# Kernel optimization log

Measured on AMD Instinct MI355X. Metric: run time of the kernel, lower is better.

The kernel has to match this reference:

```python
import jax, jax.numpy as jnp
import numpy as np

B, H, W, C = 16, 56, 56, 384
NH, WS = 12, 7
N = WS * WS
NW = (H // WS) * (W // WS)
SHIFTS = (0, WS // 2)
HD = C // NH
SCALE = HD ** -0.5


def _rel_idx():
    ch, cw = np.meshgrid(np.arange(WS), np.arange(WS), indexing='ij')
    cf = np.stack([ch.ravel(), cw.ravel()])            # (2, N)
    rc = cf[:, :, None] - cf[:, None, :]               # (2, N, N)
    rc = rc.transpose(1, 2, 0).copy()
    rc[:, :, 0] += WS - 1
    rc[:, :, 1] += WS - 1
    rc[:, :, 0] *= 2 * WS - 1
    return rc.sum(-1).astype(np.int32)                 # (N, N)


def _attn_mask(shift):
    img = np.zeros((H, W))
    sl = (slice(0, -WS), slice(-WS, -shift), slice(-shift, None))
    cnt = 0
    for hs in sl:
        for ws_ in sl:
            img[hs, ws_] = cnt
            cnt += 1
    mw = img.reshape(H // WS, WS, W // WS, WS).transpose(0, 2, 1, 3).reshape(-1, N)
    d = mw[:, None, :] - mw[:, :, None]
    return np.where(d != 0, -100.0, 0.0).astype(np.float32)  # (NW, N, N)


def setup_inputs() -> dict:
    key = jax.random.key(0)
    ks = jax.random.split(key, 8)
    p = lambda k, shape: (jax.random.normal(k, shape, jnp.float32) * 0.02)
    return dict(
        x=jax.random.normal(ks[0], (B, H, W, C), jnp.float32),
        attn_mask=jnp.asarray(_attn_mask(SHIFTS[1])),
        rel_idx=jnp.asarray(_rel_idx()),
        norm1_g=jnp.ones((2, C), jnp.float32),
        norm1_b=jnp.zeros((2, C), jnp.float32),
        qkv_w=p(ks[1], (2, 3 * C, C)),
        qkv_b=jnp.zeros((2, 3 * C), jnp.float32),
        rpb=p(ks[2], (2, (2 * WS - 1) ** 2, NH)),
        proj_w=p(ks[3], (2, C, C)),
        proj_b=jnp.zeros((2, C), jnp.float32),
        norm2_g=jnp.ones((2, C), jnp.float32),
        norm2_b=jnp.zeros((2, C), jnp.float32),
        fc1_w=p(ks[4], (2, 4 * C, C)),
        fc1_b=jnp.zeros((2, 4 * C), jnp.float32),
        fc2_w=p(ks[5], (2, C, 4 * C)),
        fc2_b=jnp.zeros((2, C), jnp.float32),
    )


def _ln(x, g, b):
    m = x.mean(-1, keepdims=True)
    v = x.var(-1, keepdims=True)
    return (x - m) * jax.lax.rsqrt(v + 1e-5) * g + b


def _partition(x):
    # (B,H,W,C) -> (B*nW, N, C)
    x = x.reshape(B, H // WS, WS, W // WS, WS, C)
    return x.transpose(0, 1, 3, 2, 4, 5).reshape(-1, N, C)


def _reverse(w):
    # (B*nW, N, C) -> (B,H,W,C)
    w = w.reshape(B, H // WS, W // WS, WS, WS, C)
    return w.transpose(0, 1, 3, 2, 4, 5).reshape(B, H, W, C)


def reference(x, attn_mask, rel_idx, norm1_g, norm1_b, qkv_w, qkv_b, rpb,
              proj_w, proj_b, norm2_g, norm2_b, fc1_w, fc1_b, fc2_w, fc2_b):
    for i, shift in enumerate(SHIFTS):
        shortcut = x.reshape(B, H * W, C)
        xn = _ln(shortcut, norm1_g[i], norm1_b[i]).reshape(B, H, W, C)
        if shift > 0:
            xn = jnp.roll(xn, (-shift, -shift), (1, 2))
        xw = _partition(xn)                               # (B_, N, C)
        qkv = xw @ qkv_w[i].T + qkv_b[i]                  # (B_, N, 3C)
        qkv = qkv.reshape(-1, N, 3, NH, HD).transpose(2, 0, 3, 1, 4)
        q, k, v = qkv[0], qkv[1], qkv[2]                  # (B_, NH, N, HD)
        attn = jnp.einsum('bhnd,bhmd->bhnm', q * SCALE, k)
        bias = rpb[i][rel_idx.reshape(-1)].reshape(N, N, NH).transpose(2, 0, 1)
        attn = attn + bias[None]
        if shift > 0:
            attn = attn.reshape(B, NW, NH, N, N) + attn_mask[None, :, None]
            attn = attn.reshape(-1, NH, N, N)
        attn = jax.nn.softmax(attn, axis=-1)
        out = jnp.einsum('bhnm,bhmd->bhnd', attn, v)
        out = out.transpose(0, 2, 1, 3).reshape(-1, N, C)
        out = out @ proj_w[i].T + proj_b[i]
        sx = _reverse(out)
        if shift > 0:
            sx = jnp.roll(sx, (shift, shift), (1, 2))
        x = shortcut + sx.reshape(B, H * W, C)
        h = jax.nn.gelu(_ln(x, norm2_g[i], norm2_b[i]) @ fc1_w[i].T + fc1_b[i],
                        approximate=False)
        x = x + (h @ fc2_w[i].T + fc2_b[i])
        x = x.reshape(B, H, W, C)
    return x
```

## Files before the change

### kernel.cpp

```cpp
#include <hip/hip_runtime.h>
#include <math.h>

typedef unsigned short u16;
typedef unsigned int   u32;
typedef __attribute__((ext_vector_type(4))) float f32x4;
typedef __attribute__((ext_vector_type(8))) short bf16x8;

#define M_TOK 50176
#define CDIM  384

__device__ __forceinline__ u16 f2b(float f){
  union { float f; u32 u; } v; v.f = f;
  u32 r = v.u + 0x7fffu + ((v.u >> 16) & 1u);
  return (u16)(r >> 16);
}
__device__ __forceinline__ u32 pack2(float a, float b){
  return (u32)f2b(a) | ((u32)f2b(b) << 16);
}

__device__ __forceinline__ void gload_lds16(const u16* g, u16* l){
  __builtin_amdgcn_global_load_lds((const __attribute__((address_space(1))) u32*)g,
                                   (__attribute__((address_space(3))) u32*)l, 16, 0, 0);
}

__global__ void cvtw(const float* __restrict__ in, u16* __restrict__ out, int n4){
  int i = blockIdx.x * 256 + threadIdx.x;
  if (i < n4){
    float4 v = ((const float4*)in)[i];
    uint2 o; o.x = pack2(v.x, v.y); o.y = pack2(v.z, v.w);
    ((uint2*)out)[i] = o;
  }
}

__global__ __launch_bounds__(256) void ln_kernel(
    const float* __restrict__ x, const float* __restrict__ g,
    const float* __restrict__ b, u16* __restrict__ out, int ntok)
{
  int wave = threadIdx.x >> 6, lane = threadIdx.x & 63;
  for (long t = blockIdx.x * 4 + wave; t < ntok; t += (long)gridDim.x * 4){
    const float* xr = x + t * CDIM;
    float v[6]; float s = 0.f, ss = 0.f;
    #pragma unroll
    for (int j = 0; j < 6; ++j){ v[j] = xr[j*64 + lane]; s += v[j]; ss += v[j]*v[j]; }
    #pragma unroll
    for (int o = 32; o >= 1; o >>= 1){ s += __shfl_xor(s, o); ss += __shfl_xor(ss, o); }
    float mean = s * (1.f/384.f);
    float var  = ss * (1.f/384.f) - mean*mean;
    float rs   = rsqrtf(var + 1e-5f);
    #pragma unroll
    for (int j = 0; j < 6; ++j){
      int c = j*64 + lane;
      out[t*CDIM + c] = f2b((v[j] - mean) * rs * g[c] + b[c]);
    }
  }
}

template<int EPI>
__global__ __launch_bounds__(256, 4) void gemm_bt(
    const u16* __restrict__ A, const u16* __restrict__ Wt,
    const float* __restrict__ bias, const float* __restrict__ resid,
    void* __restrict__ outp, int M, int N, int K)
{
  __shared__ __align__(16) u16 smem[16384];
  const int tid  = threadIdx.x;
  const int wave = tid >> 6, lane = tid & 63;
  const int nbn  = N >> 7;
  const int cpx  = gridDim.x >> 3;
  const int sid  = (blockIdx.x & 7) * cpx + (blockIdx.x >> 3);
  const int bm = sid / nbn, bn = sid % nbn;
  const int wr = wave >> 1, wc = wave & 1;
  const int l15 = lane & 15, l4 = lane >> 4;
  const int srow = tid >> 2, sch = tid & 3;

  f32x4 acc[4][4] = {};

  auto STAGE = [&](int buf, int kt){
    u16* lAp = smem + buf*4096;
    u16* lBp = smem + 8192 + buf*4096;
    #pragma unroll
    for (int it = 0; it < 2; ++it){
      int row = it*64 + srow;
      int chs = sch ^ ((srow >> 1) & 3);
      const u16* ga = A  + (size_t)(bm*128 + row) * K + kt + chs*8;
      const u16* gb = Wt + (size_t)(bn*128 + row) * K + kt + chs*8;
      gload_lds16(ga, &lAp[(it*256 + wave*64) * 8]);
      gload_lds16(gb, &lBp[(it*256 + wave*64) * 8]);
    }
  };

  const int NK = K >> 5;
  STAGE(0, 0);

  int cur = 0;
  for (int ki = 0; ki < NK; ++ki){
    if (ki + 1 < NK){
      STAGE(cur ^ 1, (ki + 1) * 32);
      asm volatile("s_waitcnt vmcnt(4)" ::: "memory");
    } else {
      asm volatile("s_waitcnt vmcnt(0)" ::: "memory");
    }
    __builtin_amdgcn_s_barrier();
    const u16* lAp = smem + cur*4096;
    const u16* lBp = smem + 8192 + cur*4096;
    bf16x8 af[4], bfr[4];
    const int rc = (l4 ^ ((l15 >> 1) & 3)) * 8;
    #pragma unroll
    for (int mi = 0; mi < 4; ++mi)
      af[mi] = *(const bf16x8*)&lAp[(wr*64 + mi*16 + l15)*32 + rc];
    #pragma unroll
    for (int ni = 0; ni < 4; ++ni)
      bfr[ni] = *(const bf16x8*)&lBp[(wc*64 + ni*16 + l15)*32 + rc];
    #pragma unroll
    for (int mi = 0; mi < 4; ++mi)
      #pragma unroll
      for (int ni = 0; ni < 4; ++ni)
        acc[mi][ni] = __builtin_amdgcn_mfma_f32_16x16x32_bf16(af[mi], bfr[ni], acc[mi][ni], 0, 0, 0);
    __builtin_amdgcn_s_barrier();
    cur ^= 1;
  }

  if (EPI == 2){
    #pragma unroll
    for (int ni = 0; ni < 4; ++ni){
      int col = bn*128 + wc*64 + ni*16 + l15;
      float bb = bias[col];
      #pragma unroll
      for (int mi = 0; mi < 4; ++mi){
        int row0 = bm*128 + wr*64 + mi*16 + l4*4;
        #pragma unroll
        for (int r = 0; r < 4; ++r){
          long off = (long)(row0 + r) * N + col;
          ((float*)outp)[off] = resid[off] + acc[mi][ni][r] + bb;
        }
      }
    }
  } else {
    #pragma unroll
    for (int ni = 0; ni < 4; ++ni){
      int colL = wc*64 + ni*16 + l15;
      float bb = bias[bn*128 + colL];
      int colS = colL ^ (l4*16);
      #pragma unroll
      for (int mi = 0; mi < 4; ++mi){
        int rowL = wr*64 + mi*16 + l4*4;
        #pragma unroll
        for (int r = 0; r < 4; ++r){
          float v = acc[mi][ni][r] + bb;
          if (EPI == 1) v = 0.5f * v * (1.f + erff(v * 0.70710678118654752f));
          smem[(rowL + r)*128 + colS] = f2b(v);
        }
      }
    }
    __syncthreads();
    const u32* eb = (const u32*)smem;
    u32* og = (u32*)outp;
    const int nW = N >> 1;
    #pragma unroll
    for (int it = 0; it < 32; ++it){
      int row = wave*32 + it;
      u32 w = eb[row*64 + (lane ^ (((row >> 2) & 3) * 8))];
      __builtin_nontemporal_store(w, &og[(size_t)(bm*128 + row) * nW + bn*64 + lane]);
    }
  }
}

__global__ void build_btbl(const float* __restrict__ rpb, const int* __restrict__ ridx,
                           float* __restrict__ btbl){
  int q = blockIdx.x & 63, h = blockIdx.x >> 6;
  int l = threadIdx.x;
  float v = -1e9f;
  if (q < 49){
    int key = (l & 3) * 16 + (l >> 2);
    if (key < 49) v = rpb[ridx[q*49 + key] * 12 + h];
  }
  btbl[(h*64 + q)*64 + l] = v;
}

template<int SHIFT>
__global__ __launch_bounds__(64) void attn_mfma(
    const u16* __restrict__ qkv,
    const float* __restrict__ btbl,
    u16* __restrict__ attn_out)
{
  __shared__ __align__(16) u16 p_lds[64*72];
  __shared__ __align__(16) u16 vt_lds[32*72];
  __shared__ int tok_lds[64];
  __shared__ int rid_lds[64];

  const int bid = blockIdx.x;
  const int h   = bid % 12;
  const int win = bid / 12;
  const int b   = win >> 6, wl = win & 63;
  const int wy  = wl >> 3,  wx = wl & 7;
  const int lane = threadIdx.x;
  const int l15 = lane & 15, l4 = lane >> 4;

  auto tokof = [&](int n)->int{
    int r = (n * 9363) >> 16;
    int c = n - r * 7;
    int hh = wy*7 + r + SHIFT; if (hh >= 56) hh -= 56;
    int ww = wx*7 + c + SHIFT; if (ww >= 56) ww -= 56;
    return b*3136 + hh*56 + ww;
  };

  {
    const int n  = lane;
    const int nc = n < 49 ? n : 48;
    const int t  = tokof(nc);
    tok_lds[n] = t;
    if (SHIFT){
      int r = (nc * 9363) >> 16, c = nc - r*7;
      int gh = wy*7 + r, gw = wx*7 + c;
      int rh = gh <= 48 ? 0 : (gh <= 52 ? 1 : 2);
      int rw = gw <= 48 ? 0 : (gw <= 52 ? 1 : 2);
      rid_lds[n] = rh*3 + rw;
    }
    const uint4* vp = (const uint4*)(qkv + (size_t)t*1152 + 768 + h*32);
    u32 w[16];
    #pragma unroll
    for (int j4 = 0; j4 < 4; ++j4){
      uint4 u = vp[j4];
      w[j4*4+0]=u.x; w[j4*4+1]=u.y; w[j4*4+2]=u.z; w[j4*4+3]=u.w;
    }
    if (n >= 49){
      #pragma unroll
      for (int j = 0; j < 16; ++j) w[j] = 0;
    }
    #pragma unroll
    for (int j = 0; j < 16; ++j){
      vt_lds[(2*j  )*72 + n] = (u16)(w[j] & 0xffffu);
      vt_lds[(2*j+1)*72 + n] = (u16)(w[j] >> 16);
    }
  }

  bf16x8 qa[4], kb[4];
  #pragma unroll
  for (int mi = 0; mi < 4; ++mi){
    int row = mi*16 + l15; int t = tokof(row < 49 ? row : 48);
    qa[mi] = *(const bf16x8*)(qkv + (size_t)t*1152 + h*32 + l4*8);
  }
  #pragma unroll
  for (int ni = 0; ni < 4; ++ni){
    int row = ni*16 + l15; int t = tokof(row < 49 ? row : 48);
    kb[ni] = *(const bf16x8*)(qkv + (size_t)t*1152 + 384 + h*32 + l4*8);
  }
  f32x4 s[4][4] = {};
  #pragma unroll
  for (int mi = 0; mi < 4; ++mi)
    #pragma unroll
    for (int ni = 0; ni < 4; ++ni)
      s[mi][ni] = __builtin_amdgcn_mfma_f32_16x16x32_bf16(qa[mi], kb[ni], s[mi][ni], 0, 0, 0);

  __syncthreads();

  int rid_k[4];
  if (SHIFT){
    #pragma unroll
    for (int ni = 0; ni < 4; ++ni) rid_k[ni] = rid_lds[ni*16 + l15];
  }

  const float* bt = btbl + h*4096;
  float den[4][4];
  #pragma unroll
  for (int mi = 0; mi < 4; ++mi){
    #pragma unroll
    for (int r = 0; r < 4; ++r){
      int q = mi*16 + l4*4 + r;
      f32x4 bq = *(const f32x4*)(bt + q*64 + l15*4);
      int ridq = 0;
      if (SHIFT) ridq = rid_lds[q];
      #pragma unroll
      for (int ni = 0; ni < 4; ++ni){
        float v = s[mi][ni][r] * 0.17677669529663687f + bq[ni];
        if (SHIFT) v += (ridq == rid_k[ni]) ? 0.f : -100.f;
        s[mi][ni][r] = v;
      }
      float m0 = fmaxf(fmaxf(s[mi][0][r], s[mi][1][r]), fmaxf(s[mi][2][r], s[mi][3][r]));
      #pragma unroll
      for (int o = 1; o <= 8; o <<= 1) m0 = fmaxf(m0, __shfl_xor(m0, o));
      float d0 = 0.f;
      #pragma unroll
      for (int ni = 0; ni < 4; ++ni){
        float e = __expf(s[mi][ni][r] - m0);
        s[mi][ni][r] = e; d0 += e;
      }
      #pragma unroll
      for (int o = 1; o <= 8; o <<= 1) d0 += __shfl_xor(d0, o);
      den[mi][r] = d0;
    }
  }

  #pragma unroll
  for (int mi = 0; mi < 4; ++mi)
    #pragma unroll
    for (int r = 0; r < 4; ++r){
      int q = mi*16 + l4*4 + r;
      #pragma unroll
      for (int ni = 0; ni < 4; ++ni)
        p_lds[q*72 + ni*16 + l15] = f2b(s[mi][ni][r]);
    }

  __syncthreads();

  f32x4 o2[4][2] = {};
  #pragma unroll
  for (int ks = 0; ks < 2; ++ks){
    bf16x8 vb[2];
    #pragma unroll
    for (int ni = 0; ni < 2; ++ni)
      vb[ni] = *(const bf16x8*)&vt_lds[(ni*16 + l15)*72 + ks*32 + l4*8];
    #pragma unroll
    for (int mi = 0; mi < 4; ++mi){
      bf16x8 pa = *(const bf16x8*)&p_lds[(mi*16 + l15)*72 + ks*32 + l4*8];
      #pragma unroll
      for (int ni = 0; ni < 2; ++ni)
        o2[mi][ni] = __builtin_amdgcn_mfma_f32_16x16x32_bf16(pa, vb[ni], o2[mi][ni], 0, 0, 0);
    }
  }

  #pragma unroll
  for (int mi = 0; mi < 4; ++mi){
    #pragma unroll
    for (int r = 0; r < 4; ++r){
      int q = mi*16 + l4*4 + r;
      if (q < 49){
        float inv = 1.f / den[mi][r];
        long t = tok_lds[q];
        #pragma unroll
        for (int ni = 0; ni < 2; ++ni){
          int d = ni*16 + l15;
          attn_out[t*384 + h*32 + d] = f2b(o2[mi][ni][r] * inv);
        }
      }
    }
  }
}

extern "C" void kernel_launch(void* const* d_in, const int* in_sizes, int n_in,
                              void* d_out, int out_size, void* d_ws, size_t ws_size,
                              hipStream_t stream)
{
  const float* x_in   = (const float*)d_in[0];
  const int*   relidx = (const int*)d_in[2];
  const float* n1g    = (const float*)d_in[3];
  const float* n1b    = (const float*)d_in[4];
  const float* qkvw   = (const float*)d_in[5];
  const float* qkvb   = (const float*)d_in[6];
  const float* rpb    = (const float*)d_in[7];
  const float* pw     = (const float*)d_in[8];
  const float* pb     = (const float*)d_in[9];
  const float* n2g    = (const float*)d_in[10];
  const float* n2b    = (const float*)d_in[11];
  const float* f1w    = (const float*)d_in[12];
  const float* f1b    = (const float*)d_in[13];
  const float* f2w    = (const float*)d_in[14];
  const float* f2bb   = (const float*)d_in[15];
  float* xout = (float*)d_out;

  char* ws = (char*)d_ws;
  u16* wqkv  = (u16*)ws; ws += (size_t)2*1152*384*2;
  u16* wproj = (u16*)ws; ws += (size_t)2*384*384*2;
  u16* wfc1  = (u16*)ws; ws += (size_t)2*1536*384*2;
  u16* wfc2  = (u16*)ws; ws += (size_t)2*384*1536*2;
  u16* bufA  = (u16*)ws; ws += (size_t)M_TOK*1536*2;
  u16* bufB  = (u16*)ws; ws += (size_t)M_TOK*384*2;
  float* btbl = (float*)(bufA + (size_t)M_TOK*1152);

  {
    int n;
    n = 2*1152*384;  cvtw<<<dim3((n/4+255)/256), dim3(256), 0, stream>>>(qkvw, wqkv, n/4);
    n = 2*384*384;   cvtw<<<dim3((n/4+255)/256), dim3(256), 0, stream>>>(pw,   wproj, n/4);
    n = 2*1536*384;  cvtw<<<dim3((n/4+255)/256), dim3(256), 0, stream>>>(f1w,  wfc1, n/4);
    n = 2*384*1536;  cvtw<<<dim3((n/4+255)/256), dim3(256), 0, stream>>>(f2w,  wfc2, n/4);
  }

  for (int i = 0; i < 2; ++i){
    const float* xi = (i == 0) ? x_in : xout;
    ln_kernel<<<dim3(2048), dim3(256), 0, stream>>>(xi, n1g + i*384, n1b + i*384, bufB, M_TOK);
    gemm_bt<0><<<dim3(3528), dim3(256), 0, stream>>>(
        bufB, wqkv + (size_t)i*1152*384, qkvb + i*1152, nullptr, bufA, M_TOK, 1152, 384);
    build_btbl<<<dim3(768), dim3(64), 0, stream>>>(rpb + (size_t)i*169*12, relidx, btbl);
    if (i == 0)
      attn_mfma<0><<<dim3(12288), dim3(64), 0, stream>>>(bufA, btbl, bufB);
    else
      attn_mfma<3><<<dim3(12288), dim3(64), 0, stream>>>(bufA, btbl, bufB);
    gemm_bt<2><<<dim3(1176), dim3(256), 0, stream>>>(
        bufB, wproj + (size_t)i*384*384, pb + i*384, xi, xout, M_TOK, 384, 384);
    ln_kernel<<<dim3(2048), dim3(256), 0, stream>>>(xout, n2g + i*384, n2b + i*384, bufB, M_TOK);
    gemm_bt<1><<<dim3(4704), dim3(256), 0, stream>>>(
        bufB, wfc1 + (size_t)i*1536*384, f1b + i*1536, nullptr, bufA, M_TOK, 1536, 384);
    gemm_bt<2><<<dim3(1176), dim3(256), 0, stream>>>(
        bufA, wfc2 + (size_t)i*384*1536, f2bb + i*384, xout, xout, M_TOK, 384, 1536);
  }
  (void)in_sizes; (void)n_in; (void)out_size; (void)ws_size;
}
```

Before: 965.0 us.

## Enlarge GEMM tile to 256x128 with triple-buffered LDS pipeline

Doubles the GEMM M-tile to 256 rows (8x4 MFMA accumulators per wave) and moves from double to triple buffering of the K-slices, with adjusted vmcnt waits. It also fixes the XCD block remap for grids not divisible by 8, halves all GEMM grid sizes, and splits the bf16 epilogue into two 128-row passes through LDS. The intent is better operand reuse per global load and deeper load latency hiding. In exchange it uses more registers and LDS, so occupancy drops (launch bounds lowered to 2 blocks per CU) and fewer workgroups are launched.

```diff
diff --git a/kernel.cpp b/kernel.cpp
--- a/kernel.cpp
+++ b/kernel.cpp
@@ -56,67 +56,76 @@
 }
 
 template<int EPI>
-__global__ __launch_bounds__(256, 4) void gemm_bt(
+__global__ __launch_bounds__(256, 2) void gemm_bt(
     const u16* __restrict__ A, const u16* __restrict__ Wt,
     const float* __restrict__ bias, const float* __restrict__ resid,
     void* __restrict__ outp, int M, int N, int K)
 {
-  __shared__ __align__(16) u16 smem[16384];
+  __shared__ __align__(16) u16 smem[3*12288];
   const int tid  = threadIdx.x;
   const int wave = tid >> 6, lane = tid & 63;
   const int nbn  = N >> 7;
-  const int cpx  = gridDim.x >> 3;
-  const int sid  = (blockIdx.x & 7) * cpx + (blockIdx.x >> 3);
+  const int nwg = gridDim.x;
+  const int q8 = nwg >> 3, r8 = nwg & 7, xcd = blockIdx.x & 7, o8 = blockIdx.x >> 3;
+  const int sid = (xcd < r8 ? xcd*(q8+1) : r8*(q8+1) + (xcd-r8)*q8) + o8;
   const int bm = sid / nbn, bn = sid % nbn;
   const int wr = wave >> 1, wc = wave & 1;
   const int l15 = lane & 15, l4 = lane >> 4;
-  const int srow = tid >> 2, sch = tid & 3;
-
-  f32x4 acc[4][4] = {};
+
+  f32x4 acc[8][4] = {};
 
   auto STAGE = [&](int buf, int kt){
-    u16* lAp = smem + buf*4096;
-    u16* lBp = smem + 8192 + buf*4096;
+    u16* lAp = smem + buf*12288;
+    u16* lBp = smem + buf*12288 + 8192;
+    #pragma unroll
+    for (int it = 0; it < 4; ++it){
+      int flat = it*256 + tid;
+      int row = flat >> 2, c = flat & 3;
+      const u16* ga = A + (size_t)(bm*256 + row) * K + kt + (c ^ ((row >> 1) & 3))*8;
+      gload_lds16(ga, &lAp[flat*8]);
+    }
     #pragma unroll
     for (int it = 0; it < 2; ++it){
-      int row = it*64 + srow;
-      int chs = sch ^ ((srow >> 1) & 3);
-      const u16* ga = A  + (size_t)(bm*128 + row) * K + kt + chs*8;
-      const u16* gb = Wt + (size_t)(bn*128 + row) * K + kt + chs*8;
-      gload_lds16(ga, &lAp[(it*256 + wave*64) * 8]);
-      gload_lds16(gb, &lBp[(it*256 + wave*64) * 8]);
+      int flat = it*256 + tid;
+      int row = flat >> 2, c = flat & 3;
+      const u16* gb = Wt + (size_t)(bn*128 + row) * K + kt + (c ^ ((row >> 1) & 3))*8;
+      gload_lds16(gb, &lBp[flat*8]);
     }
   };
 
   const int NK = K >> 5;
   STAGE(0, 0);
+  if (NK > 1) STAGE(1, 32);
 
   int cur = 0;
   for (int ki = 0; ki < NK; ++ki){
-    if (ki + 1 < NK){
-      STAGE(cur ^ 1, (ki + 1) * 32);
-      asm volatile("s_waitcnt vmcnt(4)" ::: "memory");
+    if (ki + 2 < NK){
+      int s = cur + 2; if (s >= 3) s -= 3;
+      STAGE(s, (ki + 2) * 32);
+      asm volatile("s_waitcnt vmcnt(12)" ::: "memory");
+    } else if (ki + 1 < NK){
+      asm volatile("s_waitcnt vmcnt(6)" ::: "memory");
     } else {
       asm volatile("s_waitcnt vmcnt(0)" ::: "memory");
     }
     __builtin_amdgcn_s_barrier();
-    const u16* lAp = smem + cur*4096;
-    const u16* lBp = smem + 8192 + cur*4096;
-    bf16x8 af[4], bfr[4];
+    const u16* lAp = smem + cur*12288;
+    const u16* lBp = smem + cur*12288 + 8192;
+    bf16x8 af[8], bfr[4];
     const int rc = (l4 ^ ((l15 >> 1) & 3)) * 8;
     #pragma unroll
-    for (int mi = 0; mi < 4; ++mi)
-      af[mi] = *(const bf16x8*)&lAp[(wr*64 + mi*16 + l15)*32 + rc];
+    for (int mi = 0; mi < 8; ++mi)
+      af[mi] = *(const bf16x8*)&lAp[(wr*128 + mi*16 + l15)*32 + rc];
     #pragma unroll
     for (int ni = 0; ni < 4; ++ni)
       bfr[ni] = *(const bf16x8*)&lBp[(wc*64 + ni*16 + l15)*32 + rc];
     #pragma unroll
-    for (int mi = 0; mi < 4; ++mi)
+    for (int mi = 0; mi < 8; ++mi)
       #pragma unroll
       for (int ni = 0; ni < 4; ++ni)
         acc[mi][ni] = __builtin_amdgcn_mfma_f32_16x16x32_bf16(af[mi], bfr[ni], acc[mi][ni], 0, 0, 0);
     __builtin_amdgcn_s_barrier();
-    cur ^= 1;
+    cur += 1; if (cur >= 3) cur = 0;
   }
 
   if (EPI == 2){
@@ -125,8 +134,8 @@
       int col = bn*128 + wc*64 + ni*16 + l15;
       float bb = bias[col];
       #pragma unroll
-      for (int mi = 0; mi < 4; ++mi){
-        int row0 = bm*128 + wr*64 + mi*16 + l4*4;
+      for (int mi = 0; mi < 8; ++mi){
+        int row0 = bm*256 + wr*128 + mi*16 + l4*4;
         #pragma unroll
         for (int r = 0; r < 4; ++r){
           long off = (long)(row0 + r) * N + col;
@@ -135,31 +144,37 @@
       }
     }
   } else {
-    #pragma unroll
-    for (int ni = 0; ni < 4; ++ni){
-      int colL = wc*64 + ni*16 + l15;
-      float bb = bias[bn*128 + colL];
-      int colS = colL ^ (l4*16);
-      #pragma unroll
-      for (int mi = 0; mi < 4; ++mi){
-        int rowL = wr*64 + mi*16 + l4*4;
-        #pragma unroll
-        for (int r = 0; r < 4; ++r){
-          float v = acc[mi][ni][r] + bb;
-          if (EPI == 1) v = 0.5f * v * (1.f + erff(v * 0.70710678118654752f));
-          smem[(rowL + r)*128 + colS] = f2b(v);
-        }
-      }
-    }
-    __syncthreads();
-    const u32* eb = (const u32*)smem;
     u32* og = (u32*)outp;
     const int nW = N >> 1;
     #pragma unroll
-    for (int it = 0; it < 32; ++it){
-      int row = wave*32 + it;
-      u32 w = eb[row*64 + (lane ^ (((row >> 2) & 3) * 8))];
-      __builtin_nontemporal_store(w, &og[(size_t)(bm*128 + row) * nW + bn*64 + lane]);
+    for (int h = 0; h < 2; ++h){
+      __syncthreads();
+      if (wr == h){
+        #pragma unroll
+        for (int ni = 0; ni < 4; ++ni){
+          int colL = wc*64 + ni*16 + l15;
+          float bb = bias[bn*128 + colL];
+          int colS = colL ^ (l4*16);
+          #pragma unroll
+          for (int mi = 0; mi < 8; ++mi){
+            int rowL = mi*16 + l4*4;
+            #pragma unroll
+            for (int r = 0; r < 4; ++r){
+              float v = acc[mi][ni][r] + bb;
+              if (EPI == 1) v = 0.5f * v * (1.f + erff(v * 0.70710678118654752f));
+              smem[(rowL + r)*128 + colS] = f2b(v);
+            }
+          }
+        }
+      }
+      __syncthreads();
+      const u32* eb = (const u32*)smem;
+      #pragma unroll
+      for (int it = 0; it < 32; ++it){
+        int row = wave*32 + it;
+        u32 w = eb[row*64 + (lane ^ (((row >> 2) & 3) * 8))];
+        __builtin_nontemporal_store(w, &og[(size_t)(bm*256 + h*128 + row) * nW + bn*64 + lane]);
+      }
     }
   }
 }
@@ -377,19 +392,19 @@
   for (int i = 0; i < 2; ++i){
     const float* xi = (i == 0) ? x_in : xout;
     ln_kernel<<<dim3(2048), dim3(256), 0, stream>>>(xi, n1g + i*384, n1b + i*384, bufB, M_TOK);
-    gemm_bt<0><<<dim3(3528), dim3(256), 0, stream>>>(
+    gemm_bt<0><<<dim3(1764), dim3(256), 0, stream>>>(
         bufB, wqkv + (size_t)i*1152*384, qkvb + i*1152, nullptr, bufA, M_TOK, 1152, 384);
     build_btbl<<<dim3(768), dim3(64), 0, stream>>>(rpb + (size_t)i*169*12, relidx, btbl);
     if (i == 0)
       attn_mfma<0><<<dim3(12288), dim3(64), 0, stream>>>(bufA, btbl, bufB);
     else
       attn_mfma<3><<<dim3(12288), dim3(64), 0, stream>>>(bufA, btbl, bufB);
-    gemm_bt<2><<<dim3(1176), dim3(256), 0, stream>>>(
+    gemm_bt<2><<<dim3(588), dim3(256), 0, stream>>>(
         bufB, wproj + (size_t)i*384*384, pb + i*384, xi, xout, M_TOK, 384, 384);
     ln_kernel<<<dim3(2048), dim3(256), 0, stream>>>(xout, n2g + i*384, n2b + i*384, bufB, M_TOK);
-    gemm_bt<1><<<dim3(4704), dim3(256), 0, stream>>>(
+    gemm_bt<1><<<dim3(2352), dim3(256), 0, stream>>>(
         bufB, wfc1 + (size_t)i*1536*384, f1b + i*1536, nullptr, bufA, M_TOK, 1536, 384);
-    gemm_bt<2><<<dim3(1176), dim3(256), 0, stream>>>(
+    gemm_bt<2><<<dim3(588), dim3(256), 0, stream>>>(
         bufA, wfc2 + (size_t)i*384*1536, f2bb + i*384, xout, xout, M_TOK, 384, 1536);
   }
   (void)in_sizes; (void)n_in; (void)out_size; (void)ws_size;
```

Result: slower. 1.755 ms (+81.8%).

## Run MLP GEMMs in FP8 with FP8 activations and weights

Applied to the files above, without the earlier changes.

Converts the fc1/fc2 weights, the LN2 output and the GELU hidden activations to FP8 e4m3, and adds a new FP8 MFMA GEMM kernel (16x16x32) for both MLP matmuls. This halves the bytes moved for the large hidden tensor and doubles the MFMA throughput relative to bf16. It also changes the XCD block remapping to handle grids not divisible by 8. The FP8 GEMM writes its epilogue straight to global memory byte by byte, which may give poorly coalesced stores, and unscaled e4m3 adds noticeable precision loss.

```diff
diff --git a/kernel.cpp b/kernel.cpp
--- a/kernel.cpp
+++ b/kernel.cpp
@@ -1,8 +1,11 @@
 #include <hip/hip_runtime.h>
+#include <hip/hip_fp8.h>
 #include <math.h>
 
+typedef unsigned char  u8;
 typedef unsigned short u16;
 typedef unsigned int   u32;
+typedef long long      i64;
 typedef __attribute__((ext_vector_type(4))) float f32x4;
 typedef __attribute__((ext_vector_type(8))) short bf16x8;
 
@@ -17,8 +20,12 @@
 __device__ __forceinline__ u32 pack2(float a, float b){
   return (u32)f2b(a) | ((u32)f2b(b) << 16);
 }
-
-__device__ __forceinline__ void gload_lds16(const u16* g, u16* l){
+__device__ __forceinline__ u8 f2q(float v){
+  __hip_fp8_e4m3 t(v);
+  return *reinterpret_cast<u8*>(&t);
+}
+
+__device__ __forceinline__ void gload_lds16(const void* g, void* l){
   __builtin_amdgcn_global_load_lds((const __attribute__((address_space(1))) u32*)g,
                                    (__attribute__((address_space(3))) u32*)l, 16, 0, 0);
 }
@@ -31,10 +38,20 @@
     ((uint2*)out)[i] = o;
   }
 }
-
+__global__ void cvtw8(const float* __restrict__ in, u8* __restrict__ out, int n4){
+  int i = blockIdx.x * 256 + threadIdx.x;
+  if (i < n4){
+    float4 v = ((const float4*)in)[i];
+    u32 o = (u32)f2q(v.x) | ((u32)f2q(v.y) << 8) |
+            ((u32)f2q(v.z) << 16) | ((u32)f2q(v.w) << 24);
+    ((u32*)out)[i] = o;
+  }
+}
+
+template<int F8>
 __global__ __launch_bounds__(256) void ln_kernel(
     const float* __restrict__ x, const float* __restrict__ g,
-    const float* __restrict__ b, u16* __restrict__ out, int ntok)
+    const float* __restrict__ b, void* __restrict__ out, int ntok)
 {
   int wave = threadIdx.x >> 6, lane = threadIdx.x & 63;
   for (long t = blockIdx.x * 4 + wave; t < ntok; t += (long)gridDim.x * 4){
@@ -50,7 +67,9 @@
     #pragma unroll
     for (int j = 0; j < 6; ++j){
       int c = j*64 + lane;
-      out[t*CDIM + c] = f2b((v[j] - mean) * rs * g[c] + b[c]);
+      float val = (v[j] - mean) * rs * g[c] + b[c];
+      if (F8) ((u8*)out)[t*CDIM + c] = f2q(val);
+      else    ((u16*)out)[t*CDIM + c] = f2b(val);
     }
   }
 }
@@ -65,8 +84,9 @@
   const int tid  = threadIdx.x;
   const int wave = tid >> 6, lane = tid & 63;
   const int nbn  = N >> 7;
-  const int cpx  = gridDim.x >> 3;
-  const int sid  = (blockIdx.x & 7) * cpx + (blockIdx.x >> 3);
+  const int nwg = gridDim.x;
+  const int q8 = nwg >> 3, r8 = nwg & 7, xcd = blockIdx.x & 7, o8 = blockIdx.x >> 3;
+  const int sid = (xcd < r8 ? xcd*(q8+1) : r8*(q8+1) + (xcd-r8)*q8) + o8;
   const int bm = sid / nbn, bn = sid % nbn;
   const int wr = wave >> 1, wc = wave & 1;
   const int l15 = lane & 15, l4 = lane >> 4;
@@ -146,7 +166,6 @@
         #pragma unroll
         for (int r = 0; r < 4; ++r){
           float v = acc[mi][ni][r] + bb;
-          if (EPI == 1) v = 0.5f * v * (1.f + erff(v * 0.70710678118654752f));
           smem[(rowL + r)*128 + colS] = f2b(v);
         }
       }
@@ -160,6 +179,98 @@
       int row = wave*32 + it;
       u32 w = eb[row*64 + (lane ^ (((row >> 2) & 3) * 8))];
       __builtin_nontemporal_store(w, &og[(size_t)(bm*128 + row) * nW + bn*64 + lane]);
+    }
+  }
+}
+
+template<int EPI>
+__global__ __launch_bounds__(256, 4) void gemm_f8(
+    const u8* __restrict__ A, const u8* __restrict__ Wt,
+    const float* __restrict__ bias, const float* __restrict__ resid,
+    void* __restrict__ outp, int M, int N, int K)
+{
+  __shared__ __align__(16) u8 smem[16384];
+  const int tid  = threadIdx.x;
+  const int wave = tid >> 6, lane = tid & 63;
+  const int nbn  = N >> 7;
+  const int nwg = gridDim.x;
+  const int q8 = nwg >> 3, r8 = nwg & 7, xcd = blockIdx.x & 7, o8 = blockIdx.x >> 3;
+  const int sid = (xcd < r8 ? xcd*(q8+1) : r8*(q8+1) + (xcd-r8)*q8) + o8;
+  const int bm = sid / nbn, bn = sid % nbn;
+  const int wr = wave >> 1, wc = wave & 1;
+  const int l15 = lane & 15, l4 = lane >> 4;
+  const int srow = tid >> 1, sch = tid & 1;
+
+  f32x4 acc[4][4] = {};
+
+  auto STAGE = [&](int buf, int kt){
+    const u8* ga = A  + (size_t)(bm*128 + srow) * K + kt + sch*16;
+    const u8* gb = Wt + (size_t)(bn*128 + srow) * K + kt + sch*16;
+    gload_lds16(ga, &smem[buf*8192 + tid*16]);
+    gload_lds16(gb, &smem[buf*8192 + 4096 + tid*16]);
+  };
+
+  const int NK = K >> 5;
+  STAGE(0, 0);
+
+  int cur = 0;
+  for (int ki = 0; ki < NK; ++ki){
+    if (ki + 1 < NK){
+      STAGE(cur ^ 1, (ki + 1) * 32);
+      asm volatile("s_waitcnt vmcnt(2)" ::: "memory");
+    } else {
+      asm volatile("s_waitcnt vmcnt(0)" ::: "memory");
+    }
+    __builtin_amdgcn_s_barrier();
+    const u8* lAp = smem + cur*8192;
+    const u8* lBp = smem + cur*8192 + 4096;
+    i64 af[4], bf[4];
+    #pragma unroll
+    for (int mi = 0; mi < 4; ++mi)
+      af[mi] = *(const i64*)&lAp[(wr*64 + mi*16 + l15)*32 + l4*8];
+    #pragma unroll
+    for (int ni = 0; ni < 4; ++ni)
+      bf[ni] = *(const i64*)&lBp[(wc*64 + ni*16 + l15)*32 + l4*8];
+    #pragma unroll
+    for (int mi = 0; mi < 4; ++mi)
+      #pragma unroll
+      for (int ni = 0; ni < 4; ++ni)
+        acc[mi][ni] = __builtin_amdgcn_mfma_f32_16x16x32_fp8_fp8(af[mi], bf[ni], acc[mi][ni], 0, 0, 0);
+    __builtin_amdgcn_s_barrier();
+    cur ^= 1;
+  }
+
+  if (EPI == 2){
+    #pragma unroll
+    for (int ni = 0; ni < 4; ++ni){
+      int col = bn*128 + wc*64 + ni*16 + l15;
+      float bb = bias[col];
+      #pragma unroll
+      for (int mi = 0; mi < 4; ++mi){
+        int row0 = bm*128 + wr*64 + mi*16 + l4*4;
+        #pragma unroll
+        for (int r = 0; r < 4; ++r){
+          long off = (long)(row0 + r) * N + col;
+          ((float*)outp)[off] = resid[off] + acc[mi][ni][r] + bb;
+        }
+      }
+    }
+  } else {
+    u8* og = (u8*)outp;
+    #pragma unroll
+    for (int ni = 0; ni < 4; ++ni){
+      int col = bn*128 + wc*64 + ni*16 + l15;
+      float bb = bias[col];
+      #pragma unroll
+      for (int mi = 0; mi < 4; ++mi){
+        int row0 = bm*128 + wr*64 + mi*16 + l4*4;
+        #pragma unroll
+        for (int r = 0; r < 4; ++r){
+          float v = acc[mi][ni][r] + bb;
+          v = 0.5f * v * (1.f + erff(v * 0.70710678118654752f));
+          og[(size_t)(row0 + r) * N + col] = f2q(v);
+        }
+      }
     }
   }
 }
@@ -178,8 +289,7 @@
 
 template<int SHIFT>
 __global__ __launch_bounds__(64) void attn_mfma(
-    const u16* __restrict__ qkv,
-    const float* __restrict__ btbl,
+    const u16* __restrict__ qkv, const float* __restrict__ btbl,
     u16* __restrict__ attn_out)
 {
   __shared__ __align__(16) u16 p_lds[64*72];
@@ -358,25 +468,27 @@
   float* xout = (float*)d_out;
 
   char* ws = (char*)d_ws;
-  u16* wqkv  = (u16*)ws; ws += (size_t)2*1152*384*2;
-  u16* wproj = (u16*)ws; ws += (size_t)2*384*384*2;
-  u16* wfc1  = (u16*)ws; ws += (size_t)2*1536*384*2;
-  u16* wfc2  = (u16*)ws; ws += (size_t)2*384*1536*2;
-  u16* bufA  = (u16*)ws; ws += (size_t)M_TOK*1536*2;
-  u16* bufB  = (u16*)ws; ws += (size_t)M_TOK*384*2;
+  u16* wqkv   = (u16*)ws; ws += (size_t)2*1152*384*2;
+  u16* wproj  = (u16*)ws; ws += (size_t)2*384*384*2;
+  u8*  wfc1q  = (u8*)ws;  ws += (size_t)2*1536*384;
+  u8*  wfc2q  = (u8*)ws;  ws += (size_t)2*384*1536;
+  u16* bufA   = (u16*)ws; ws += (size_t)M_TOK*1536*2;
+  u16* bufB   = (u16*)ws; ws += (size_t)M_TOK*384*2;
+  u8*  bufD   = (u8*)ws;  ws += (size_t)M_TOK*384;
   float* btbl = (float*)(bufA + (size_t)M_TOK*1152);
+  u8* h8 = (u8*)bufA;
 
   {
     int n;
-    n = 2*1152*384;  cvtw<<<dim3((n/4+255)/256), dim3(256), 0, stream>>>(qkvw, wqkv, n/4);
-    n = 2*384*384;   cvtw<<<dim3((n/4+255)/256), dim3(256), 0, stream>>>(pw,   wproj, n/4);
-    n = 2*1536*384;  cvtw<<<dim3((n/4+255)/256), dim3(256), 0, stream>>>(f1w,  wfc1, n/4);
-    n = 2*384*1536;  cvtw<<<dim3((n/4+255)/256), dim3(256), 0, stream>>>(f2w,  wfc2, n/4);
+    n = 2*1152*384;  cvtw <<<dim3((n/4+255)/256), dim3(256), 0, stream>>>(qkvw, wqkv,  n/4);
+    n = 2*384*384;   cvtw <<<dim3((n/4+255)/256), dim3(256), 0, stream>>>(pw,   wproj, n/4);
+    n = 2*1536*384;  cvtw8<<<dim3((n/4+255)/256), dim3(256), 0, stream>>>(f1w,  wfc1q, n/4);
+    n = 2*384*1536;  cvtw8<<<dim3((n/4+255)/256), dim3(256), 0, stream>>>(f2w,  wfc2q, n/4);
   }
 
   for (int i = 0; i < 2; ++i){
     const float* xi = (i == 0) ? x_in : xout;
-    ln_kernel<<<dim3(2048), dim3(256), 0, stream>>>(xi, n1g + i*384, n1b + i*384, bufB, M_TOK);
+    ln_kernel<0><<<dim3(2048), dim3(256), 0, stream>>>(xi, n1g + i*384, n1b + i*384, bufB, M_TOK);
     gemm_bt<0><<<dim3(3528), dim3(256), 0, stream>>>(
         bufB, wqkv + (size_t)i*1152*384, qkvb + i*1152, nullptr, bufA, M_TOK, 1152, 384);
     build_btbl<<<dim3(768), dim3(64), 0, stream>>>(rpb + (size_t)i*169*12, relidx, btbl);
@@ -386,11 +498,11 @@
       attn_mfma<3><<<dim3(12288), dim3(64), 0, stream>>>(bufA, btbl, bufB);
     gemm_bt<2><<<dim3(1176), dim3(256), 0, stream>>>(
         bufB, wproj + (size_t)i*384*384, pb + i*384, xi, xout, M_TOK, 384, 384);
-    ln_kernel<<<dim3(2048), dim3(256), 0, stream>>>(xout, n2g + i*384, n2b + i*384, bufB, M_TOK);
-    gemm_bt<1><<<dim3(4704), dim3(256), 0, stream>>>(
-        bufB, wfc1 + (size_t)i*1536*384, f1b + i*1536, nullptr, bufA, M_TOK, 1536, 384);
-    gemm_bt<2><<<dim3(1176), dim3(256), 0, stream>>>(
-        bufA, wfc2 + (size_t)i*384*1536, f2bb + i*384, xout, xout, M_TOK, 384, 1536);
+    ln_kernel<1><<<dim3(2048), dim3(256), 0, stream>>>(xout, n2g + i*384, n2b + i*384, bufD, M_TOK);
+    gemm_f8<1><<<dim3(4704), dim3(256), 0, stream>>>(
+        bufD, wfc1q + (size_t)i*1536*384, f1b + i*1536, nullptr, h8, M_TOK, 1536, 384);
+    gemm_f8<2><<<dim3(1176), dim3(256), 0, stream>>>(
+        h8, wfc2q + (size_t)i*384*1536, f2bb + i*384, xout, xout, M_TOK, 384, 1536);
   }
   (void)in_sizes; (void)n_in; (void)out_size; (void)ws_size;
 }
```

Measured after the change: 957.0 us. Within noise of the previous version (-0.8%).
